# Optimization experiments

Hardware: AMD Instinct MI355X
Metric: run time of the kernel (lower is better)

## Reference

```python
import jax, jax.numpy as jnp
import numpy as np

DIM = 512
NUM_HEADS = 8
HEAD_DIM = DIM // NUM_HEADS
EPS = 1e-12  # F.normalize eps


def _l2norm(x):
    # F.normalize(x, dim=-1): x / max(||x||, eps)
    n = jnp.sqrt(jnp.sum(x * x, axis=-1, keepdims=True))
    return x / jnp.maximum(n, EPS)


def setup_inputs() -> dict:
    key = jax.random.key(0)
    ks = jax.random.split(key, 5)
    B, T, D = 4, 2048, DIM
    z = jax.random.normal(ks[0], (B, T, D), dtype=jnp.float32)
    t = jnp.zeros((1,), dtype=jnp.float32)  # unused ODE time
    omega = jax.random.normal(ks[1], (1, 1, D), dtype=jnp.float32) * 0.1
    # nn.Linear default init scale ~ U(-1/sqrt(fan_in), 1/sqrt(fan_in))
    s = 1.0 / np.sqrt(D)
    W_qk = jax.random.uniform(ks[2], (2 * D, D), jnp.float32, -s, s)
    W_out = jax.random.uniform(ks[3], (D, D), jnp.float32, -s, s)
    b_out = jax.random.uniform(ks[4], (D,), jnp.float32, -s, s)
    return {"t": t, "z": z, "omega": omega, "W_qk": W_qk, "W_out": W_out, "b_out": b_out}


def reference(t, z, omega, W_qk, W_out, b_out):
    B, T, D = z.shape
    H, hd = NUM_HEADS, HEAD_DIM
    qk = z @ W_qk.T                      # [B,T,2D]
    q, k = qk[..., :D], qk[..., D:]
    q = _l2norm(q.reshape(B, T, H, hd))  # [B,T,H,hd]
    k = _l2norm(k.reshape(B, T, H, hd))
    # coupling: [B,H,T,T]
    coupling = jnp.einsum("bqhd,bkhd->bhqk", q, k)
    interaction = jnp.sin(coupling)
    force = jnp.einsum("bhqk,bkhd->bqhd", interaction, k).reshape(B, T, D)
    return omega + force @ W_out.T + b_out
```

## Files before the change

### kernel.cpp

```cpp
#include <hip/hip_runtime.h>
#include <hip/hip_bf16.h>

typedef unsigned short u16;
typedef _Float16 f16;
typedef __attribute__((ext_vector_type(8))) _Float16 f16x8;
typedef __attribute__((ext_vector_type(2))) __fp16 h16x2;
typedef __attribute__((ext_vector_type(8))) short short8;
typedef __attribute__((ext_vector_type(4))) float f32x4;

#define B_ 4
#define T_ 2048
#define D_ 512
#define H_ 8
#define M_ (B_*T_)
#define INV2PI 0.15915494309189535f

__device__ f16 g_qb[M_*D_];
__device__ f16 g_kb[M_*D_];
__device__ f16 g_kTp[(size_t)B_*H_*64*T_];
__device__ f16 g_fA[(size_t)M_*D_];
__device__ f16 g_fB[(size_t)M_*D_];

__device__ inline float sin2pi(float x) {
#if __has_builtin(__builtin_amdgcn_sinf)
  return __builtin_amdgcn_sinf(x);
#else
  return __sinf(x * 6.283185307179586f);
#endif
}

__device__ inline f16x8 cvt8h(f32x4 a, f32x4 b) {
  union { h16x2 h[4]; f16x8 v; } u;
  u.h[0] = __builtin_amdgcn_cvt_pkrtz(a[0], a[1]);
  u.h[1] = __builtin_amdgcn_cvt_pkrtz(a[2], a[3]);
  u.h[2] = __builtin_amdgcn_cvt_pkrtz(b[0], b[1]);
  u.h[3] = __builtin_amdgcn_cvt_pkrtz(b[2], b[3]);
  return u.v;
}

__device__ inline int perm5(int p) {
  int lg = p >> 3, e = p & 7;
  return (e < 4) ? lg*4 + e : 16 + lg*4 + (e & 3);
}

template<int MODE>
__global__ __launch_bounds__(256, 2)
void gemm_bt(float* __restrict__ Cout, const float* __restrict__ add1,
             const float* __restrict__ add2, const float* __restrict__ Afp,
             const float* __restrict__ Bfp) {
  constexpr int K = 512;
  constexpr int N = (MODE == 0) ? 1024 : 512;
  constexpr int NB = N/128;
  __shared__ f16 As[128*72];
  __shared__ f16 Bs[128*72];
  const int bidx = blockIdx.x;
  const int xcd = bidx & 7, idx = bidx >> 3;
  const int mp = xcd + 8*(idx/NB);
  const int np = idx % NB;
  const int m0 = mp*128, n0 = np*128;
  const int t = threadIdx.x;
  const int w = t>>6, l = t&63;
  const int wr = (w>>1)*64, wc = (w&1)*64;
  const int lg = l>>4, li = l&15;
  const int srow = t>>3, scol = (t&7)*8;

  f32x4 acc[4][4] = {};

  for (int k0 = 0; k0 < K; k0 += 64) {
#pragma unroll
    for (int p = 0; p < 4; ++p) {
      int r = srow + p*32;
      {
        f32x4 b0 = *(const f32x4*)&Bfp[(size_t)(n0+r)*K + k0 + scol];
        f32x4 b1 = *(const f32x4*)&Bfp[(size_t)(n0+r)*K + k0 + scol + 4];
        *(f16x8*)&Bs[r*72 + scol] = cvt8h(b0, b1);
      }
      if (MODE == 0) {
        f32x4 a0 = *(const f32x4*)&Afp[(size_t)(m0+r)*K + k0 + scol];
        f32x4 a1 = *(const f32x4*)&Afp[(size_t)(m0+r)*K + k0 + scol + 4];
        *(f16x8*)&As[r*72 + scol] = cvt8h(a0, a1);
      } else {
        f16x8 a = *(const f16x8*)&g_fA[(size_t)(m0+r)*K + k0 + scol];
        f16x8 c = *(const f16x8*)&g_fB[(size_t)(m0+r)*K + k0 + scol];
        *(f16x8*)&As[r*72 + scol] = a + c;
      }
    }
    __syncthreads();
#pragma unroll
    for (int ks = 0; ks < 2; ++ks) {
      f16x8 af[4], bf[4];
#pragma unroll
      for (int i = 0; i < 4; ++i)
        af[i] = *(const f16x8*)&As[(wr + i*16 + li)*72 + ks*32 + lg*8];
#pragma unroll
      for (int j = 0; j < 4; ++j)
        bf[j] = *(const f16x8*)&Bs[(wc + j*16 + li)*72 + ks*32 + lg*8];
#pragma unroll
      for (int i = 0; i < 4; ++i)
#pragma unroll
        for (int j = 0; j < 4; ++j)
          acc[i][j] = __builtin_amdgcn_mfma_f32_16x16x32_f16(af[i], bf[j], acc[i][j], 0, 0, 0);
    }
    __syncthreads();
  }

  if (MODE == 0) {
    const bool isq = (n0 < 512);
    f16* dst = isq ? g_qb : g_kb;
    const float qs = isq ? INV2PI : 1.0f;
    const int nb = (isq ? n0 : n0 - 512) + wc;
#pragma unroll
    for (int i = 0; i < 4; ++i) {
#pragma unroll
      for (int r = 0; r < 4; ++r) {
        float s = 0.f;
#pragma unroll
        for (int j = 0; j < 4; ++j) s += acc[i][j][r]*acc[i][j][r];
#pragma unroll
        for (int off = 1; off < 16; off <<= 1) s += __shfl_xor(s, off);
        float sc = qs / fmaxf(sqrtf(s), 1e-12f);
        int row = m0 + wr + i*16 + lg*4 + r;
#pragma unroll
        for (int j = 0; j < 4; ++j)
          dst[(size_t)row*D_ + nb + j*16 + li] = (f16)(acc[i][j][r]*sc);
      }
    }
  } else {
#pragma unroll
    for (int i = 0; i < 4; ++i) {
#pragma unroll
      for (int j = 0; j < 4; ++j) {
        int col = n0 + wc + j*16 + li;
        float badd = add1[col] + add2[col];
#pragma unroll
        for (int r = 0; r < 4; ++r) {
          int row = m0 + wr + i*16 + lg*4 + r;
          Cout[(size_t)row*N + col] = acc[i][j][r] + badd;
        }
      }
    }
  }
}

__global__ void transpose_k_kernel() {
  __shared__ u16 tile[64*72];
  const int t0 = blockIdx.x*64, bh = blockIdx.y;
  const int b = bh>>3, h = bh&7;
  const int t = threadIdx.x;
  const u16* kb = (const u16*)g_kb;
  u16* kT = (u16*)g_kTp;
  {
    int r = t>>2, cs = (t&3)*16;
    const u16* src = kb + (size_t)(b*T_ + t0 + r)*D_ + h*64 + cs;
    *(short8*)&tile[r*72 + cs]     = *(const short8*)(src);
    *(short8*)&tile[r*72 + cs + 8] = *(const short8*)(src + 8);
  }
  __syncthreads();
  {
    int d = t>>2, ts = (t&3)*16;
    short8 o0, o1;
#pragma unroll
    for (int j = 0; j < 8; ++j) {
      int p0 = ts + j, p1 = ts + 8 + j;
      int s0 = (p0 & ~31) | perm5(p0 & 31);
      int s1 = (p1 & ~31) | perm5(p1 & 31);
      o0[j] = (short)tile[s0*72 + d];
      o1[j] = (short)tile[s1*72 + d];
    }
    u16* dst = kT + ((size_t)bh*64 + d)*T_ + t0 + ts;
    *(short8*)(dst)     = o0;
    *(short8*)(dst + 8) = o1;
  }
}

__global__ __launch_bounds__(256, 2)
void kuramoto_attn_kernel() {
  __shared__ u16 Ks[2][128*72];
  __shared__ u16 KTs[2][64*136];
  const int wg  = blockIdx.x;
  const int wgp = (wg & 7)*64 + (wg >> 3);
  const int bh = wgp >> 4, qt = (wgp & 15) >> 1, kh = wgp & 1;
  const int b = bh >> 3, h = bh & 7;
  const int t = threadIdx.x;
  const int w = t>>6, l = t&63;
  const int lg = l>>4, li = l&15;

  f16x8 bq[2][4];
#pragma unroll
  for (int ks = 0; ks < 2; ++ks)
#pragma unroll
    for (int j = 0; j < 4; ++j)
      bq[ks][j] = *(const f16x8*)&g_qb[(size_t)(b*T_ + qt*256 + w*64 + j*16 + li)*D_
                                       + h*64 + ks*32 + lg*8];

  const int sr = t>>3, sc = (t&7)*8;
  const int sd = t>>4, sk = (t&15)*8;
  const u16* kbase = (const u16*)g_kb  + (size_t)b*T_*D_ + h*64;
  const u16* tbase = (const u16*)g_kTp + (size_t)bh*64*T_;
  const int kt0 = kh*8;

  f32x4 acc_o[4][4] = {};

#pragma unroll
  for (int p = 0; p < 4; ++p) {
    *(short8*)&Ks[0][(sr + p*32)*72 + sc] =
      *(const short8*)&kbase[(size_t)(kt0*128 + sr + p*32)*D_ + sc];
    *(short8*)&KTs[0][(sd + p*16)*136 + sk] =
      *(const short8*)&tbase[(size_t)(sd + p*16)*T_ + kt0*128 + sk];
  }
  __syncthreads();

#define QK_STEP(KKP, S) do {                                                   \
  _Pragma("unroll") for (int ks = 0; ks < 2; ++ks) {                           \
    f16x8 af0 = *(const f16x8*)&Ks[buf][((2*(KKP)  )*16 + li)*72 + ks*32 + lg*8]; \
    f16x8 af1 = *(const f16x8*)&Ks[buf][((2*(KKP)+1)*16 + li)*72 + ks*32 + lg*8]; \
    __builtin_amdgcn_s_setprio(1);                                             \
    _Pragma("unroll") for (int j = 0; j < 4; ++j) {                            \
      S[0][j] = __builtin_amdgcn_mfma_f32_16x16x32_f16(af0, bq[ks][j], S[0][j], 0,0,0); \
      S[1][j] = __builtin_amdgcn_mfma_f32_16x16x32_f16(af1, bq[ks][j], S[1][j], 0,0,0); \
    }                                                                          \
    __builtin_amdgcn_s_setprio(0); } } while(0)

#define SINPV_STEP(KKP, S) do {                                                \
  f16x8 apv[4];                                                                \
  _Pragma("unroll") for (int j = 0; j < 4; ++j) {                              \
    union { h16x2 h[4]; f16x8 v; } cv;                                         \
    cv.h[0] = __builtin_amdgcn_cvt_pkrtz(sin2pi(S[0][j][0]), sin2pi(S[0][j][1])); \
    cv.h[1] = __builtin_amdgcn_cvt_pkrtz(sin2pi(S[0][j][2]), sin2pi(S[0][j][3])); \
    cv.h[2] = __builtin_amdgcn_cvt_pkrtz(sin2pi(S[1][j][0]), sin2pi(S[1][j][1])); \
    cv.h[3] = __builtin_amdgcn_cvt_pkrtz(sin2pi(S[1][j][2]), sin2pi(S[1][j][3])); \
    apv[j] = cv.v; }                                                           \
  _Pragma("unroll") for (int di = 0; di < 4; ++di) {                           \
    f16x8 bv = *(const f16x8*)&KTs[buf][(di*16 + li)*136 + (KKP)*32 + lg*8];   \
    __builtin_amdgcn_s_setprio(1);                                             \
    _Pragma("unroll") for (int j = 0; j < 4; ++j)                              \
      acc_o[j][di] = __builtin_amdgcn_mfma_f32_16x16x32_f16(apv[j], bv, acc_o[j][di], 0,0,0); \
    __builtin_amdgcn_s_setprio(0);                                             \
  } } while(0)

#pragma unroll 2
  for (int ii = 0; ii < 8; ++ii) {
    const int buf = ii & 1;
    short8 rk[4], rt[4];
    if (ii < 7) {
      const int ktn = kt0 + ii + 1;
#pragma unroll
      for (int p = 0; p < 4; ++p) {
        rk[p] = *(const short8*)&kbase[(size_t)(ktn*128 + sr + p*32)*D_ + sc];
        rt[p] = *(const short8*)&tbase[(size_t)(sd + p*16)*T_ + ktn*128 + sk];
      }
    }

    f32x4 sA[2][4] = {};
    f32x4 sB[2][4] = {};
    QK_STEP(0, sA);
    QK_STEP(1, sB);  SINPV_STEP(0, sA);
#pragma unroll
    for (int z = 0; z < 2; ++z)
#pragma unroll
      for (int j = 0; j < 4; ++j) sA[z][j] = (f32x4)(0.f);
    QK_STEP(2, sA);  SINPV_STEP(1, sB);
#pragma unroll
    for (int z = 0; z < 2; ++z)
#pragma unroll
      for (int j = 0; j < 4; ++j) sB[z][j] = (f32x4)(0.f);
    QK_STEP(3, sB);  SINPV_STEP(2, sA);
                     SINPV_STEP(3, sB);

    if (ii < 7) {
#pragma unroll
      for (int p = 0; p < 4; ++p) {
        *(short8*)&Ks[buf^1][(sr + p*32)*72 + sc] = rk[p];
        *(short8*)&KTs[buf^1][(sd + p*16)*136 + sk] = rt[p];
      }
    }
    __syncthreads();
  }
#undef QK_STEP
#undef SINPV_STEP

  f16* F = kh ? g_fB : g_fA;
#pragma unroll
  for (int j = 0; j < 4; ++j)
#pragma unroll
    for (int di = 0; di < 4; ++di)
#pragma unroll
      for (int r = 0; r < 4; ++r) {
        int row = b*T_ + qt*256 + w*64 + j*16 + lg*4 + r;
        int col = h*64 + di*16 + li;
        F[(size_t)row*D_ + col] = (f16)acc_o[j][di][r];
      }
}

extern "C" void kernel_launch(void* const* d_in, const int* in_sizes, int n_in,
                              void* d_out, int out_size, void* d_ws, size_t ws_size,
                              hipStream_t stream) {
  const float* z     = (const float*)d_in[1];
  const float* omega = (const float*)d_in[2];
  const float* Wqk   = (const float*)d_in[3];
  const float* Wout  = (const float*)d_in[4];
  const float* bout  = (const float*)d_in[5];
  float* out = (float*)d_out;

  gemm_bt<0><<<512, 256, 0, stream>>>(nullptr, nullptr, nullptr, z, Wqk);
  transpose_k_kernel<<<dim3(T_/64, B_*H_), 256, 0, stream>>>();
  kuramoto_attn_kernel<<<512, 256, 0, stream>>>();
  gemm_bt<1><<<256, 256, 0, stream>>>(out, omega, bout, nullptr, Wout);
}
```

Baseline: 163.9 us.

## Use direct global-to-LDS loads with XOR swizzle in attention; simplify GEMM grid

Replaces register-staged prefetch of K and K^T tiles in the attention kernel with global_load_lds direct-to-LDS loads into unpadded, XOR-swizzled shared buffers, with fragment reads adjusted to match. This frees registers and avoids separate LDS store instructions, and the swizzle keeps bank conflicts low without padding. The GEMM kernels drop the XCD-aware block index remapping in favor of a plain 2D grid, which may change L2 locality across chiplets.

```diff
diff --git a/kernel.cpp b/kernel.cpp
--- a/kernel.cpp
+++ b/kernel.cpp
@@ -27,6 +27,12 @@
 #else
   return __sinf(x * 6.283185307179586f);
 #endif
+}
+
+__device__ inline void gload16(const void* g, void* l) {
+  __builtin_amdgcn_global_load_lds(
+      (const __attribute__((address_space(1))) unsigned int*)g,
+      (__attribute__((address_space(3))) unsigned int*)l, 16, 0, 0);
 }
 
 __device__ inline f16x8 cvt8h(f32x4 a, f32x4 b) {
@@ -50,14 +56,9 @@
              const float* __restrict__ Bfp) {
   constexpr int K = 512;
   constexpr int N = (MODE == 0) ? 1024 : 512;
-  constexpr int NB = N/128;
   __shared__ f16 As[128*72];
   __shared__ f16 Bs[128*72];
-  const int bidx = blockIdx.x;
-  const int xcd = bidx & 7, idx = bidx >> 3;
-  const int mp = xcd + 8*(idx/NB);
-  const int np = idx % NB;
-  const int m0 = mp*128, n0 = np*128;
+  const int m0 = blockIdx.x*128, n0 = blockIdx.y*128;
   const int t = threadIdx.x;
   const int w = t>>6, l = t&63;
   const int wr = (w>>1)*64, wc = (w&1)*64;
@@ -175,8 +176,8 @@
 
 __global__ __launch_bounds__(256, 2)
 void kuramoto_attn_kernel() {
-  __shared__ u16 Ks[2][128*72];
-  __shared__ u16 KTs[2][64*136];
+  __shared__ f16 Ks[2][128*64];
+  __shared__ f16 KTs[2][64*128];
   const int wg  = blockIdx.x;
   const int wgp = (wg & 7)*64 + (wg >> 3);
   const int bh = wgp >> 4, qt = (wgp & 15) >> 1, kh = wgp & 1;
@@ -193,27 +194,32 @@
       bq[ks][j] = *(const f16x8*)&g_qb[(size_t)(b*T_ + qt*256 + w*64 + j*16 + li)*D_
                                        + h*64 + ks*32 + lg*8];
 
-  const int sr = t>>3, sc = (t&7)*8;
-  const int sd = t>>4, sk = (t&15)*8;
-  const u16* kbase = (const u16*)g_kb  + (size_t)b*T_*D_ + h*64;
-  const u16* tbase = (const u16*)g_kTp + (size_t)bh*64*T_;
+  const f16* kbase = g_kb  + (size_t)b*T_*D_ + h*64;
+  const f16* tbase = g_kTp + (size_t)bh*64*T_;
   const int kt0 = kh*8;
 
+#define STAGE(BUFI, KT) do {                                                   \
+  _Pragma("unroll") for (int p = 0; p < 4; ++p) {                              \
+    int idx = (w*4+p)*64 + l;                                                  \
+    int rK = idx >> 3, sK = idx & 7;                                           \
+    gload16(&kbase[(size_t)((KT)*128 + rK)*D_ + ((sK ^ (rK & 7))<<3)],         \
+            &Ks[BUFI][(w*4+p)*512]);                                           \
+    int rT = idx >> 4, sT = idx & 15;                                          \
+    gload16(&tbase[(size_t)rT*T_ + (KT)*128 + ((sT ^ (rT & 15))<<3)],          \
+            &KTs[BUFI][(w*4+p)*512]);                                          \
+  } } while(0)
+
   f32x4 acc_o[4][4] = {};
 
-#pragma unroll
-  for (int p = 0; p < 4; ++p) {
-    *(short8*)&Ks[0][(sr + p*32)*72 + sc] =
-      *(const short8*)&kbase[(size_t)(kt0*128 + sr + p*32)*D_ + sc];
-    *(short8*)&KTs[0][(sd + p*16)*136 + sk] =
-      *(const short8*)&tbase[(size_t)(sd + p*16)*T_ + kt0*128 + sk];
-  }
+  STAGE(0, kt0);
   __syncthreads();
 
 #define QK_STEP(KKP, S) do {                                                   \
   _Pragma("unroll") for (int ks = 0; ks < 2; ++ks) {                           \
-    f16x8 af0 = *(const f16x8*)&Ks[buf][((2*(KKP)  )*16 + li)*72 + ks*32 + lg*8]; \
-    f16x8 af1 = *(const f16x8*)&Ks[buf][((2*(KKP)+1)*16 + li)*72 + ks*32 + lg*8]; \
+    f16x8 af0 = *(const f16x8*)&Ks[buf][((2*(KKP)  )*16 + li)*64               \
+                                        + (((ks*4+lg) ^ (li&7))<<3)];          \
+    f16x8 af1 = *(const f16x8*)&Ks[buf][((2*(KKP)+1)*16 + li)*64               \
+                                        + (((ks*4+lg) ^ (li&7))<<3)];          \
     __builtin_amdgcn_s_setprio(1);                                             \
     _Pragma("unroll") for (int j = 0; j < 4; ++j) {                            \
       S[0][j] = __builtin_amdgcn_mfma_f32_16x16x32_f16(af0, bq[ks][j], S[0][j], 0,0,0); \
@@ -231,7 +237,8 @@
     cv.h[3] = __builtin_amdgcn_cvt_pkrtz(sin2pi(S[1][j][2]), sin2pi(S[1][j][3])); \
     apv[j] = cv.v; }                                                           \
   _Pragma("unroll") for (int di = 0; di < 4; ++di) {                           \
-    f16x8 bv = *(const f16x8*)&KTs[buf][(di*16 + li)*136 + (KKP)*32 + lg*8];   \
+    f16x8 bv = *(const f16x8*)&KTs[buf][(di*16 + li)*128                       \
+                                        + ((((KKP)*4+lg) ^ li)<<3)];           \
     __builtin_amdgcn_s_setprio(1);                                             \
     _Pragma("unroll") for (int j = 0; j < 4; ++j)                              \
       acc_o[j][di] = __builtin_amdgcn_mfma_f32_16x16x32_f16(apv[j], bv, acc_o[j][di], 0,0,0); \
@@ -241,15 +248,7 @@
 #pragma unroll 2
   for (int ii = 0; ii < 8; ++ii) {
     const int buf = ii & 1;
-    short8 rk[4], rt[4];
-    if (ii < 7) {
-      const int ktn = kt0 + ii + 1;
-#pragma unroll
-      for (int p = 0; p < 4; ++p) {
-        rk[p] = *(const short8*)&kbase[(size_t)(ktn*128 + sr + p*32)*D_ + sc];
-        rt[p] = *(const short8*)&tbase[(size_t)(sd + p*16)*T_ + ktn*128 + sk];
-      }
-    }
+    if (ii < 7) STAGE(buf^1, kt0 + ii + 1);
 
     f32x4 sA[2][4] = {};
     f32x4 sB[2][4] = {};
@@ -267,17 +266,11 @@
     QK_STEP(3, sB);  SINPV_STEP(2, sA);
                      SINPV_STEP(3, sB);
 
-    if (ii < 7) {
-#pragma unroll
-      for (int p = 0; p < 4; ++p) {
-        *(short8*)&Ks[buf^1][(sr + p*32)*72 + sc] = rk[p];
-        *(short8*)&KTs[buf^1][(sd + p*16)*136 + sk] = rt[p];
-      }
-    }
     __syncthreads();
   }
 #undef QK_STEP
 #undef SINPV_STEP
+#undef STAGE
 
   f16* F = kh ? g_fB : g_fA;
 #pragma unroll
@@ -302,8 +295,8 @@
   const float* bout  = (const float*)d_in[5];
   float* out = (float*)d_out;
 
-  gemm_bt<0><<<512, 256, 0, stream>>>(nullptr, nullptr, nullptr, z, Wqk);
+  gemm_bt<0><<<dim3(M_/128, 1024/128), 256, 0, stream>>>(nullptr, nullptr, nullptr, z, Wqk);
   transpose_k_kernel<<<dim3(T_/64, B_*H_), 256, 0, stream>>>();
   kuramoto_attn_kernel<<<512, 256, 0, stream>>>();
-  gemm_bt<1><<<256, 256, 0, stream>>>(out, omega, bout, nullptr, Wout);
-}
+  gemm_bt<1><<<dim3(M_/128, 512/128), 256, 0, stream>>>(out, omega, bout, nullptr, Wout);
+}
```

After: 153.1 us. 1.07x faster.
